# Optimization experiments

Measured on AMD Instinct MI355X. Metric: run time of the kernel, lower is better.

The kernel has to match this reference:

```python
import jax, jax.numpy as jnp
import numpy as np

T, B, H = 2048, 64, 256   # time, batch, hidden/input/memory size
A = 256                   # attention_size
IN = H + H                # cell input size = input_size + memory_size = 512
NEG = -1e12


def setup_inputs() -> dict:
    key = jax.random.key(0)
    ks = jax.random.split(key, 12)
    s = lambda k, shape, fan: jax.random.normal(k, shape, jnp.float32) / np.sqrt(fan)
    inp = {
        "input": jax.random.normal(ks[0], (B, H), jnp.float32),
        "memory": jax.random.normal(ks[1], (T, B, H), jnp.float32),
        "memory_mask": jax.random.bernoulli(ks[2], 0.9, (T, B)),
        "state": jax.random.normal(ks[3], (B, H), jnp.float32),
        # attention MLP: Linear(input+state+memory -> A, no bias), Tanh, Linear(A -> 1, no bias)
        "W_a1": s(ks[4], (H + H + H, A), H * 3),
        "w_a2": s(ks[5], (A,), A),
        # gate: Linear(IN -> IN, no bias) + sigmoid
        "W_gate": s(ks[6], (IN, IN), IN),
        # GRUCell params (torch layout: [3H, in], gates order r,z,n)
        "W_ih": s(ks[7], (3 * H, IN), IN),
        "W_hh": s(ks[8], (3 * H, H), H),
        "b_ih": jnp.zeros((3 * H,), jnp.float32),
        "b_hh": jnp.zeros((3 * H,), jnp.float32),
    }
    return inp


def reference(input, memory, memory_mask, state, W_a1, w_a2, W_gate, W_ih, W_hh, b_ih, b_hh):
    # --- additive attention: tanh(W1 @ [input, state, memory]) @ w2 ---
    # split W_a1 by the concat layout [input | state | memory]
    qs = jnp.concatenate([input, state], axis=-1) @ W_a1[: 2 * H]      # [B, A]
    mp = jnp.einsum("tbh,ha->tba", memory, W_a1[2 * H :])               # [T, B, A]
    logits = jnp.tanh(qs[None] + mp) @ w_a2                              # [T, B]
    logits = jnp.where(memory_mask, logits, NEG)
    scores = jax.nn.softmax(logits, axis=0)                              # [T, B]
    attn_vec = jnp.einsum("tb,tbh->bh", scores, memory)                  # [B, H]

    # --- gate ---
    new_input = jnp.concatenate([input, attn_vec], axis=-1)              # [B, 2H]
    gated = new_input * jax.nn.sigmoid(new_input @ W_gate)

    # --- GRU cell (torch semantics, gates r, z, n) ---
    gi = gated @ W_ih.T + b_ih                                           # [B, 3H]
    gh = state @ W_hh.T + b_hh                                           # [B, 3H]
    i_r, i_z, i_n = jnp.split(gi, 3, axis=-1)
    h_r, h_z, h_n = jnp.split(gh, 3, axis=-1)
    r = jax.nn.sigmoid(i_r + h_r)
    z = jax.nn.sigmoid(i_z + h_z)
    n = jnp.tanh(i_n + r * h_n)
    return (1.0 - z) * n + z * state                                     # [B, H]
```

## Files before the change

### kernel.cpp

```cpp
#include <hip/hip_runtime.h>
#include <hip/hip_bf16.h>

#define B_DIM 64
#define H_DIM 256
#define NCHG 4
#define CHUNKS 8
#define TCH 64
#define NEG_INF -1e12f

typedef __attribute__((ext_vector_type(8))) short short8;
typedef __attribute__((ext_vector_type(4))) float f32x4;

__device__ __forceinline__ unsigned short bfbits(float f) {
    __hip_bfloat16 h = __float2bfloat16(f);
    unsigned short u;
    __builtin_memcpy(&u, &h, 2);
    return u;
}
__device__ __forceinline__ float fast_tanh(float x) {
    float e = __expf(2.0f * x);
    return 1.0f - 2.0f / (e + 1.0f);
}
__device__ __forceinline__ float fast_sigmoid(float x) {
    return 1.0f / (1.0f + __expf(-x));
}

__global__ void prep_qs_kernel(const float* __restrict__ W_a1,
                               const float* __restrict__ input,
                               const float* __restrict__ state,
                               unsigned short* __restrict__ WmT,
                               float* __restrict__ qs) {
    __shared__ float cat[512];
    int bid = blockIdx.x, tid = threadIdx.x;
    if (bid < 256) {
        WmT[tid * 256 + bid] = bfbits(W_a1[(512 + bid) * 256 + tid]);
    } else {
        int b = bid - 256;
        cat[tid] = input[b * 256 + tid];
        cat[256 + tid] = state[b * 256 + tid];
        __syncthreads();
        int a = tid;
        float s0 = 0.f, s1 = 0.f, s2 = 0.f, s3 = 0.f;
        #pragma unroll 4
        for (int k = 0; k < 512; k += 4) {
            s0 += cat[k]     * W_a1[(k)     * 256 + a];
            s1 += cat[k + 1] * W_a1[(k + 1) * 256 + a];
            s2 += cat[k + 2] * W_a1[(k + 2) * 256 + a];
            s3 += cat[k + 3] * W_a1[(k + 3) * 256 + a];
        }
        qs[b * 256 + a] = (s0 + s1) + (s2 + s3);
    }
}

__global__ __launch_bounds__(512, 2) void attn_kernel(
    const float* __restrict__ memory, const int* __restrict__ mask,
    const unsigned short* __restrict__ WmT,
    const float* __restrict__ qs, const float* __restrict__ w_a2,
    float* __restrict__ part_m, float* __restrict__ part_l,
    float* __restrict__ part_acc)
{
    extern __shared__ char smem[];
    unsigned short* slab0 = (unsigned short*)smem;
    unsigned short* slab1 = (unsigned short*)(smem + 32768);
    float* lpart = (float*)(smem + 65536);
    int*   maskL = (int*)(smem + 65536 + 2048);

    int b = blockIdx.x, g = blockIdx.y;
    int tid = threadIdx.x;
    int lane = tid & 63, w = tid >> 6;
    int lr = lane & 15, lh = lane >> 4;
    int tbase = g * (CHUNKS * TCH);
    const float* mbase = memory + (size_t)tbase * (B_DIM * H_DIM) + b * H_DIM;

    float4 ld[8];
    #pragma unroll
    for (int i = 0; i < 8; ++i)
        ld[i] = *((const float4*)(mbase + (size_t)(i * 8 + w) * (B_DIM * H_DIM)) + lane);

    int wa0 = w * 32;
    short8 areg[8][2];
    #pragma unroll
    for (int kk = 0; kk < 8; ++kk)
        #pragma unroll
        for (int mf = 0; mf < 2; ++mf)
            areg[kk][mf] = *(const short8*)(WmT + (wa0 + mf * 16 + lr) * 256 + kk * 32 + lh * 8);

    float qv[2][4], wv[2][4];
    #pragma unroll
    for (int mf = 0; mf < 2; ++mf)
        #pragma unroll
        for (int r = 0; r < 4; ++r) {
            int a = wa0 + mf * 16 + lh * 4 + r;
            qv[mf][r] = qs[b * 256 + a];
            wv[mf][r] = w_a2[a];
        }

    maskL[tid] = mask[(tbase + tid) * B_DIM + b];

    int wby = (lane * 8) ^ (w << 4);
    #pragma unroll
    for (int i = 0; i < 8; ++i) {
        ushort4 o;
        o.x = bfbits(ld[i].x); o.y = bfbits(ld[i].y);
        o.z = bfbits(ld[i].z); o.w = bfbits(ld[i].w);
        *(ushort4*)((char*)slab0 + (i * 8 + w) * 512 + wby) = o;
    }
    __syncthreads();

    float a8[8] = {0.f, 0.f, 0.f, 0.f, 0.f, 0.f, 0.f, 0.f};
    float M = -3.4e38f, L = 0.f;
    int slice4 = ((lane >> 5) + 2 * w) * 4;
    int hpvb = (lane & 31) * 16;

    for (int s = 0; s < CHUNKS; ++s) {
        const char* cur = (const char*)((s & 1) ? slab1 : slab0);
        char* nxt = (char*)((s & 1) ? slab0 : slab1);

        if (s < CHUNKS - 1) {
            #pragma unroll
            for (int i = 0; i < 8; ++i) {
                int row = (s + 1) * TCH + i * 8 + w;
                ld[i] = *((const float4*)(mbase + (size_t)row * (B_DIM * H_DIM)) + lane);
            }
        }

        f32x4 acc[2][4];
        #pragma unroll
        for (int mf = 0; mf < 2; ++mf)
            #pragma unroll
            for (int nf = 0; nf < 4; ++nf)
                acc[mf][nf] = (f32x4){0.f, 0.f, 0.f, 0.f};
        #pragma unroll
        for (int kk = 0; kk < 8; ++kk) {
            int kbyte = kk * 64 + lh * 16;
            #pragma unroll
            for (int nf = 0; nf < 4; ++nf) {
                int t = nf * 16 + lr;
                int sw = kbyte ^ ((t & 7) << 4);
                short8 bfr = *(const short8*)(cur + t * 512 + sw);
                acc[0][nf] = __builtin_amdgcn_mfma_f32_16x16x32_bf16(areg[kk][0], bfr, acc[0][nf], 0, 0, 0);
                acc[1][nf] = __builtin_amdgcn_mfma_f32_16x16x32_bf16(areg[kk][1], bfr, acc[1][nf], 0, 0, 0);
            }
        }

        #pragma unroll
        for (int nf = 0; nf < 4; ++nf) {
            float sv = 0.f;
            #pragma unroll
            for (int mf = 0; mf < 2; ++mf)
                #pragma unroll
                for (int r = 0; r < 4; ++r)
                    sv += wv[mf][r] * fast_tanh(qv[mf][r] + acc[mf][nf][r]);
            sv += __shfl_xor(sv, 16);
            sv += __shfl_xor(sv, 32);
            if (lh == 0) lpart[w * 64 + nf * 16 + lr] = sv;
        }
        __syncthreads();

        float lg = 0.f;
        #pragma unroll
        for (int ww = 0; ww < 8; ++ww) lg += lpart[ww * 64 + lane];
        lg = maskL[s * 64 + lane] ? lg : NEG_INF;
        float mx = lg;
        #pragma unroll
        for (int d = 1; d < 64; d <<= 1) mx = fmaxf(mx, __shfl_xor(mx, d));
        float ex = __expf(lg - mx);
        float sm = ex;
        #pragma unroll
        for (int d = 1; d < 64; d <<= 1) sm += __shfl_xor(sm, d);

        float newM = fmaxf(M, mx);
        float fo = __expf(M - newM);
        L = L * fo + sm * __expf(mx - newM);
        M = newM;
        #pragma unroll
        for (int j = 0; j < 8; ++j) a8[j] *= fo;
        float pself = __expf(lg - M);

        #pragma unroll
        for (int tt = 0; tt < 4; ++tt) {
            int tl = slice4 + tt;
            float pt = __shfl(pself, tl);
            int swb = hpvb ^ ((tl & 7) << 4);
            uint4 u = *(const uint4*)(cur + tl * 512 + swb);
            a8[0] += pt * __uint_as_float(u.x << 16);
            a8[1] += pt * __uint_as_float(u.x & 0xFFFF0000u);
            a8[2] += pt * __uint_as_float(u.y << 16);
            a8[3] += pt * __uint_as_float(u.y & 0xFFFF0000u);
            a8[4] += pt * __uint_as_float(u.z << 16);
            a8[5] += pt * __uint_as_float(u.z & 0xFFFF0000u);
            a8[6] += pt * __uint_as_float(u.w << 16);
            a8[7] += pt * __uint_as_float(u.w & 0xFFFF0000u);
        }

        if (s < CHUNKS - 1) {
            #pragma unroll
            for (int i = 0; i < 8; ++i) {
                ushort4 o;
                o.x = bfbits(ld[i].x); o.y = bfbits(ld[i].y);
                o.z = bfbits(ld[i].z); o.w = bfbits(ld[i].w);
                *(ushort4*)(nxt + (i * 8 + w) * 512 + wby) = o;
            }
        }
        __syncthreads();
    }

    float* acc2 = (float*)smem;
    int oct = lane & 31, slice = 2 * w + (lane >> 5), h0 = oct * 8;
    *(float4*)(&acc2[slice * 256 + h0])     = (float4){a8[0], a8[1], a8[2], a8[3]};
    *(float4*)(&acc2[slice * 256 + h0 + 4]) = (float4){a8[4], a8[5], a8[6], a8[7]};
    __syncthreads();
    int pidx = g * B_DIM + b;
    if (tid < 256) {
        float ssum = 0.f;
        #pragma unroll
        for (int sl = 0; sl < 16; ++sl) ssum += acc2[sl * 256 + tid];
        part_acc[(size_t)pidx * 256 + tid] = ssum;
    }
    if (tid == 0) { part_m[pidx] = M; part_l[pidx] = L; }
}

__global__ void mergegate_kernel(const float* __restrict__ part_m,
                                 const float* __restrict__ part_l,
                                 const float* __restrict__ part_acc,
                                 const float* __restrict__ input,
                                 const float* __restrict__ W_gate,
                                 float* __restrict__ gated) {
    __shared__ float ni[512];
    int b = blockIdx.x, tid = threadIdx.x;
    if (tid >= 256) {
        int k = tid - 256;
        ni[k] = input[b * 256 + k];
    } else {
        int h = tid;
        float M = -3.4e38f;
        #pragma unroll
        for (int c = 0; c < NCHG; ++c) M = fmaxf(M, part_m[c * 64 + b]);
        float L = 0.f, s = 0.f;
        #pragma unroll
        for (int c = 0; c < NCHG; ++c) {
            float sc = __expf(part_m[c * 64 + b] - M);
            L += part_l[c * 64 + b] * sc;
            s += sc * part_acc[(size_t)(c * 64 + b) * 256 + h];
        }
        ni[256 + h] = s / L;
    }
    __syncthreads();
    int j = tid;
    float s0 = 0.f, s1 = 0.f, s2 = 0.f, s3 = 0.f;
    #pragma unroll 4
    for (int k = 0; k < 512; k += 4) {
        s0 += ni[k]     * W_gate[(k)     * 512 + j];
        s1 += ni[k + 1] * W_gate[(k + 1) * 512 + j];
        s2 += ni[k + 2] * W_gate[(k + 2) * 512 + j];
        s3 += ni[k + 3] * W_gate[(k + 3) * 512 + j];
    }
    float s = (s0 + s1) + (s2 + s3);
    gated[b * 512 + j] = ni[j] * fast_sigmoid(s);
}

__global__ __launch_bounds__(768) void gru_kernel(
    const float* __restrict__ gated, const float* __restrict__ state,
    const float* __restrict__ W_ih, const float* __restrict__ W_hh,
    const float* __restrict__ b_ih, const float* __restrict__ b_hh,
    float* __restrict__ out) {
    __shared__ float ld_g[4][512];
    __shared__ float ld_s[4][256];
    __shared__ float xi[3][16][4];
    __shared__ float xh[3][16][4];
    int ht = blockIdx.x & 15, bt = blockIdx.x >> 4;
    int tid = threadIdx.x;
    #pragma unroll
    for (int i = 0; i < 3; ++i) {
        int idx = i * 768 + tid;
        if (idx < 2048) ld_g[idx >> 9][idx & 511] = gated[(bt * 4 + (idx >> 9)) * 512 + (idx & 511)];
    }
    #pragma unroll
    for (int i = 0; i < 2; ++i) {
        int idx = i * 768 + tid;
        if (idx < 1024) ld_s[idx >> 8][idx & 255] = state[(bt * 4 + (idx >> 8)) * 256 + (idx & 255)];
    }

    int gid = tid >> 4, lk = tid & 15;
    int gate = gid >> 4, hl = gid & 15;
    int j = gate * 256 + ht * 16 + hl;

    float4 wi[8], wh[4];
    #pragma unroll
    for (int it = 0; it < 8; ++it)
        wi[it] = *(const float4*)(W_ih + (size_t)j * 512 + it * 64 + lk * 4);
    #pragma unroll
    for (int it = 0; it < 4; ++it)
        wh[it] = *(const float4*)(W_hh + (size_t)j * 256 + it * 64 + lk * 4);
    float bi = b_ih[j], bh = b_hh[j];
    __syncthreads();

    #pragma unroll
    for (int bb = 0; bb < 4; ++bb) {
        float g0 = 0.f, g1 = 0.f;
        #pragma unroll
        for (int it = 0; it < 8; ++it) {
            float4 gv = *(const float4*)(&ld_g[bb][it * 64 + lk * 4]);
            g0 += wi[it].x * gv.x + wi[it].z * gv.z;
            g1 += wi[it].y * gv.y + wi[it].w * gv.w;
        }
        float h0 = 0.f, h1 = 0.f;
        #pragma unroll
        for (int it = 0; it < 4; ++it) {
            float4 sv = *(const float4*)(&ld_s[bb][it * 64 + lk * 4]);
            h0 += wh[it].x * sv.x + wh[it].z * sv.z;
            h1 += wh[it].y * sv.y + wh[it].w * sv.w;
        }
        float gi_ = g0 + g1, gh_ = h0 + h1;
        #pragma unroll
        for (int m = 1; m < 16; m <<= 1) {
            gi_ += __shfl_xor(gi_, m);
            gh_ += __shfl_xor(gh_, m);
        }
        if (lk == 0) { xi[gate][hl][bb] = gi_ + bi; xh[gate][hl][bb] = gh_ + bh; }
    }
    __syncthreads();
    if (tid < 64) {
        int bb = tid >> 4, hl2 = tid & 15;
        float ir = xi[0][hl2][bb], hr = xh[0][hl2][bb];
        float iz = xi[1][hl2][bb], hz = xh[1][hl2][bb];
        float in_ = xi[2][hl2][bb], hn = xh[2][hl2][bb];
        float r = fast_sigmoid(ir + hr);
        float z = fast_sigmoid(iz + hz);
        float n = fast_tanh(in_ + r * hn);
        out[(bt * 4 + bb) * 256 + ht * 16 + hl2] =
            (1.f - z) * n + z * ld_s[bb][ht * 16 + hl2];
    }
}

extern "C" void kernel_launch(void* const* d_in, const int* in_sizes, int n_in,
                              void* d_out, int out_size, void* d_ws, size_t ws_size,
                              hipStream_t stream) {
    const float* input  = (const float*)d_in[0];
    const float* memory = (const float*)d_in[1];
    const int*   mask   = (const int*)d_in[2];
    const float* state  = (const float*)d_in[3];
    const float* W_a1   = (const float*)d_in[4];
    const float* w_a2   = (const float*)d_in[5];
    const float* W_gate = (const float*)d_in[6];
    const float* W_ih   = (const float*)d_in[7];
    const float* W_hh   = (const float*)d_in[8];
    const float* b_ih   = (const float*)d_in[9];
    const float* b_hh   = (const float*)d_in[10];
    float* out = (float*)d_out;

    char* ws = (char*)d_ws;
    unsigned short* WmT = (unsigned short*)(ws + 0);
    float* qs       = (float*)(ws + 131072);
    float* gated    = (float*)(ws + 196608);
    float* part_m   = (float*)(ws + 327680);
    float* part_l   = (float*)(ws + 331776);
    float* part_acc = (float*)(ws + 335872);

    prep_qs_kernel<<<320, 256, 0, stream>>>(W_a1, input, state, WmT, qs);

    (void)hipFuncSetAttribute((const void*)attn_kernel,
                              hipFuncAttributeMaxDynamicSharedMemorySize, 69632);
    attn_kernel<<<dim3(B_DIM, NCHG), 512, 69632, stream>>>(
        memory, mask, WmT, qs, w_a2, part_m, part_l, part_acc);

    mergegate_kernel<<<64, 512, 0, stream>>>(part_m, part_l, part_acc, input, W_gate, gated);
    gru_kernel<<<256, 768, 0, stream>>>(gated, state, W_ih, W_hh, b_ih, b_hh, out);
}
```

Baseline: 85.29 us.

## Tile attention over contiguous memory rows and drop online-softmax max tracking

Result: slower. 97.93 us (+14.8%).

```diff
diff --git a/kernel.cpp b/kernel.cpp
--- a/kernel.cpp
+++ b/kernel.cpp
@@ -3,9 +3,9 @@
 
 #define B_DIM 64
 #define H_DIM 256
-#define NCHG 4
-#define CHUNKS 8
-#define TCH 64
+#define NG 256
+#define SUBS 8
+#define RCH 64
 #define NEG_INF -1e12f
 
 typedef __attribute__((ext_vector_type(8))) short short8;
@@ -56,26 +56,27 @@
     const float* __restrict__ memory, const int* __restrict__ mask,
     const unsigned short* __restrict__ WmT,
     const float* __restrict__ qs, const float* __restrict__ w_a2,
-    float* __restrict__ part_m, float* __restrict__ part_l,
-    float* __restrict__ part_acc)
+    float* __restrict__ part_l, float* __restrict__ part_acc)
 {
     extern __shared__ char smem[];
     unsigned short* slab0 = (unsigned short*)smem;
     unsigned short* slab1 = (unsigned short*)(smem + 32768);
-    float* lpart = (float*)(smem + 65536);
-    int*   maskL = (int*)(smem + 65536 + 2048);
-
-    int b = blockIdx.x, g = blockIdx.y;
+    float* qsT   = (float*)(smem + 65536);
+    float* lpart = (float*)(smem + 65536 + 66560);
+    int*   maskL = (int*)(smem + 65536 + 66560 + 2048);
+
+    int g = blockIdx.x;
     int tid = threadIdx.x;
     int lane = tid & 63, w = tid >> 6;
     int lr = lane & 15, lh = lane >> 4;
-    int tbase = g * (CHUNKS * TCH);
-    const float* mbase = memory + (size_t)tbase * (B_DIM * H_DIM) + b * H_DIM;
-
-    float4 ld[8];
-    #pragma unroll
-    for (int i = 0; i < 8; ++i)
-        ld[i] = *((const float4*)(mbase + (size_t)(i * 8 + w) * (B_DIM * H_DIM)) + lane);
+    const float* mbase = memory + (size_t)g * (512 * H_DIM);
+
+    #pragma unroll
+    for (int i = 0; i < 32; ++i) {
+        int idx = i * 512 + tid;
+        qsT[(idx & 255) * 65 + (idx >> 8)] = qs[idx];
+    }
+    maskL[tid] = mask[g * 512 + tid];
 
     int wa0 = w * 32;
     short8 areg[8][2];
@@ -85,18 +86,17 @@
         for (int mf = 0; mf < 2; ++mf)
             areg[kk][mf] = *(const short8*)(WmT + (wa0 + mf * 16 + lr) * 256 + kk * 32 + lh * 8);
 
-    float qv[2][4], wv[2][4];
+    float wv[2][4];
     #pragma unroll
     for (int mf = 0; mf < 2; ++mf)
         #pragma unroll
-        for (int r = 0; r < 4; ++r) {
-            int a = wa0 + mf * 16 + lh * 4 + r;
-            qv[mf][r] = qs[b * 256 + a];
-            wv[mf][r] = w_a2[a];
-        }
-
-    maskL[tid] = mask[(tbase + tid) * B_DIM + b];
-
+        for (int r = 0; r < 4; ++r)
+            wv[mf][r] = w_a2[wa0 + mf * 16 + lh * 4 + r];
+
+    float4 ld[8];
+    #pragma unroll
+    for (int i = 0; i < 8; ++i)
+        ld[i] = *((const float4*)(mbase + (size_t)(i * 8 + w) * H_DIM) + lane);
     int wby = (lane * 8) ^ (w << 4);
     #pragma unroll
     for (int i = 0; i < 8; ++i) {
@@ -107,21 +107,19 @@
     }
     __syncthreads();
 
-    float a8[8] = {0.f, 0.f, 0.f, 0.f, 0.f, 0.f, 0.f, 0.f};
-    float M = -3.4e38f, L = 0.f;
-    int slice4 = ((lane >> 5) + 2 * w) * 4;
-    int hpvb = (lane & 31) * 16;
-
-    for (int s = 0; s < CHUNKS; ++s) {
+    float a32[32];
+    #pragma unroll
+    for (int j = 0; j < 32; ++j) a32[j] = 0.f;
+    float l_acc = 0.f;
+
+    for (int s = 0; s < SUBS; ++s) {
         const char* cur = (const char*)((s & 1) ? slab1 : slab0);
         char* nxt = (char*)((s & 1) ? slab0 : slab1);
 
-        if (s < CHUNKS - 1) {
-            #pragma unroll
-            for (int i = 0; i < 8; ++i) {
-                int row = (s + 1) * TCH + i * 8 + w;
-                ld[i] = *((const float4*)(mbase + (size_t)row * (B_DIM * H_DIM)) + lane);
-            }
+        if (s < SUBS - 1) {
+            #pragma unroll
+            for (int i = 0; i < 8; ++i)
+                ld[i] = *((const float4*)(mbase + (size_t)((s + 1) * RCH + i * 8 + w) * H_DIM) + lane);
         }
 
         f32x4 acc[2][4];
@@ -143,57 +141,7 @@
             }
         }
 
-        #pragma unroll
-        for (int nf = 0; nf < 4; ++nf) {
-            float sv = 0.f;
-            #pragma unroll
-            for (int mf = 0; mf < 2; ++mf)
-                #pragma unroll
-                for (int r = 0; r < 4; ++r)
-                    sv += wv[mf][r] * fast_tanh(qv[mf][r] + acc[mf][nf][r]);
-            sv += __shfl_xor(sv, 16);
-            sv += __shfl_xor(sv, 32);
-            if (lh == 0) lpart[w * 64 + nf * 16 + lr] = sv;
-        }
-        __syncthreads();
-
-        float lg = 0.f;
-        #pragma unroll
-        for (int ww = 0; ww < 8; ++ww) lg += lpart[ww * 64 + lane];
-        lg = maskL[s * 64 + lane] ? lg : NEG_INF;
-        float mx = lg;
-        #pragma unroll
-        for (int d = 1; d < 64; d <<= 1) mx = fmaxf(mx, __shfl_xor(mx, d));
-        float ex = __expf(lg - mx);
-        float sm = ex;
-        #pragma unroll
-        for (int d = 1; d < 64; d <<= 1) sm += __shfl_xor(sm, d);
-
-        float newM = fmaxf(M, mx);
-        float fo = __expf(M - newM);
-        L = L * fo + sm * __expf(mx - newM);
-        M = newM;
-        #pragma unroll
-        for (int j = 0; j < 8; ++j) a8[j] *= fo;
-        float pself = __expf(lg - M);
-
-        #pragma unroll
-        for (int tt = 0; tt < 4; ++tt) {
-            int tl = slice4 + tt;
-            float pt = __shfl(pself, tl);
-            int swb = hpvb ^ ((tl & 7) << 4);
-            uint4 u = *(const uint4*)(cur + tl * 512 + swb);
-            a8[0] += pt * __uint_as_float(u.x << 16);
-            a8[1] += pt * __uint_as_float(u.x & 0xFFFF0000u);
-            a8[2] += pt * __uint_as_float(u.y << 16);
-            a8[3] += pt * __uint_as_float(u.y & 0xFFFF0000u);
-            a8[4] += pt * __uint_as_float(u.z << 16);
-            a8[5] += pt * __uint_as_float(u.z & 0xFFFF0000u);
-            a8[6] += pt * __uint_as_float(u.w << 16);
-            a8[7] += pt * __uint_as_float(u.w & 0xFFFF0000u);
-        }
-
-        if (s < CHUNKS - 1) {
+        if (s < SUBS - 1) {
             #pragma unroll
             for (int i = 0; i < 8; ++i) {
                 ushort4 o;
@@ -202,47 +150,81 @@
                 *(ushort4*)(nxt + (i * 8 + w) * 512 + wby) = o;
             }
         }
+
+        #pragma unroll
+        for (int nf = 0; nf < 4; ++nf) {
+            int brow = nf * 16 + lr;
+            float sv = 0.f;
+            #pragma unroll
+            for (int mf = 0; mf < 2; ++mf)
+                #pragma unroll
+                for (int r = 0; r < 4; ++r) {
+                    int a = wa0 + mf * 16 + lh * 4 + r;
+                    sv += wv[mf][r] * fast_tanh(qsT[a * 65 + brow] + acc[mf][nf][r]);
+                }
+            sv += __shfl_xor(sv, 16);
+            sv += __shfl_xor(sv, 32);
+            if (lh == 0) lpart[w * 64 + brow] = sv;
+        }
         __syncthreads();
-    }
-
-    float* acc2 = (float*)smem;
-    int oct = lane & 31, slice = 2 * w + (lane >> 5), h0 = oct * 8;
-    *(float4*)(&acc2[slice * 256 + h0])     = (float4){a8[0], a8[1], a8[2], a8[3]};
-    *(float4*)(&acc2[slice * 256 + h0 + 4]) = (float4){a8[4], a8[5], a8[6], a8[7]};
-    __syncthreads();
-    int pidx = g * B_DIM + b;
-    if (tid < 256) {
-        float ssum = 0.f;
-        #pragma unroll
-        for (int sl = 0; sl < 16; ++sl) ssum += acc2[sl * 256 + tid];
-        part_acc[(size_t)pidx * 256 + tid] = ssum;
-    }
-    if (tid == 0) { part_m[pidx] = M; part_l[pidx] = L; }
-}
-
-__global__ void mergegate_kernel(const float* __restrict__ part_m,
-                                 const float* __restrict__ part_l,
+
+        float lg = 0.f;
+        #pragma unroll
+        for (int ww = 0; ww < 8; ++ww) lg += lpart[ww * 64 + lane];
+        float p = maskL[s * 64 + lane] ? __expf(lg) : 0.f;
+        if (w == 0) l_acc += p;
+
+        #pragma unroll
+        for (int j = 0; j < 4; ++j) {
+            int swb = (w * 64 + j * 16) ^ ((lane & 7) << 4);
+            uint4 u = *(const uint4*)(cur + lane * 512 + swb);
+            a32[j * 8 + 0] += p * __uint_as_float(u.x << 16);
+            a32[j * 8 + 1] += p * __uint_as_float(u.x & 0xFFFF0000u);
+            a32[j * 8 + 2] += p * __uint_as_float(u.y << 16);
+            a32[j * 8 + 3] += p * __uint_as_float(u.y & 0xFFFF0000u);
+            a32[j * 8 + 4] += p * __uint_as_float(u.z << 16);
+            a32[j * 8 + 5] += p * __uint_as_float(u.z & 0xFFFF0000u);
+            a32[j * 8 + 6] += p * __uint_as_float(u.w << 16);
+            a32[j * 8 + 7] += p * __uint_as_float(u.w & 0xFFFF0000u);
+        }
+        __syncthreads();
+    }
+
+    float* acc2 = qsT;
+    #pragma unroll
+    for (int j4 = 0; j4 < 8; ++j4)
+        *(float4*)(&acc2[lane * 257 + w * 32 + j4 * 4]) =
+            (float4){a32[j4 * 4 + 0], a32[j4 * 4 + 1], a32[j4 * 4 + 2], a32[j4 * 4 + 3]};
+    __syncthreads();
+    int hh = tid & 255, bq = tid >> 8;
+    for (int bb = bq; bb < 64; bb += 2)
+        part_acc[((size_t)bb * NG + g) * 256 + hh] = acc2[bb * 257 + hh];
+    if (w == 0) part_l[lane * NG + g] = l_acc;
+}
+
+__global__ void mergegate_kernel(const float* __restrict__ part_l,
                                  const float* __restrict__ part_acc,
                                  const float* __restrict__ input,
                                  const float* __restrict__ W_gate,
                                  float* __restrict__ gated) {
     __shared__ float ni[512];
+    __shared__ float lbuf[256];
     int b = blockIdx.x, tid = threadIdx.x;
-    if (tid >= 256) {
-        int k = tid - 256;
-        ni[k] = input[b * 256 + k];
+    if (tid < 256) lbuf[tid] = part_l[b * NG + tid];
+    __syncthreads();
+    for (int off = 128; off > 0; off >>= 1) {
+        if (tid < off) lbuf[tid] += lbuf[tid + off];
+        __syncthreads();
+    }
+    float L = lbuf[0];
+    if (tid < 256) {
+        ni[tid] = input[b * 256 + tid];
     } else {
-        int h = tid;
-        float M = -3.4e38f;
-        #pragma unroll
-        for (int c = 0; c < NCHG; ++c) M = fmaxf(M, part_m[c * 64 + b]);
-        float L = 0.f, s = 0.f;
-        #pragma unroll
-        for (int c = 0; c < NCHG; ++c) {
-            float sc = __expf(part_m[c * 64 + b] - M);
-            L += part_l[c * 64 + b] * sc;
-            s += sc * part_acc[(size_t)(c * 64 + b) * 256 + h];
-        }
+        int h = tid - 256;
+        const float* pa = part_acc + (size_t)b * NG * 256 + h;
+        float s = 0.f;
+        #pragma unroll 8
+        for (int g2 = 0; g2 < NG; ++g2) s += pa[(size_t)g2 * 256];
         ni[256 + h] = s / L;
     }
     __syncthreads();
@@ -353,17 +335,16 @@
     unsigned short* WmT = (unsigned short*)(ws + 0);
     float* qs       = (float*)(ws + 131072);
     float* gated    = (float*)(ws + 196608);
-    float* part_m   = (float*)(ws + 327680);
-    float* part_l   = (float*)(ws + 331776);
-    float* part_acc = (float*)(ws + 335872);
+    float* part_l   = (float*)(ws + 327680);
+    float* part_acc = (float*)(ws + 393216);
 
     prep_qs_kernel<<<320, 256, 0, stream>>>(W_a1, input, state, WmT, qs);
 
     (void)hipFuncSetAttribute((const void*)attn_kernel,
-                              hipFuncAttributeMaxDynamicSharedMemorySize, 69632);
-    attn_kernel<<<dim3(B_DIM, NCHG), 512, 69632, stream>>>(
-        memory, mask, WmT, qs, w_a2, part_m, part_l, part_acc);
-
-    mergegate_kernel<<<64, 512, 0, stream>>>(part_m, part_l, part_acc, input, W_gate, gated);
+                              hipFuncAttributeMaxDynamicSharedMemorySize, 136192);
+    attn_kernel<<<NG, 512, 136192, stream>>>(
+        memory, mask, WmT, qs, w_a2, part_l, part_acc);
+
+    mergegate_kernel<<<64, 512, 0, stream>>>(part_l, part_acc, input, W_gate, gated);
     gru_kernel<<<256, 768, 0, stream>>>(gated, state, W_ih, W_hh, b_ih, b_hh, out);
 }
```
